# Performance work log

Hardware: AMD Instinct MI355X
Metric: run time of the kernel (lower is better)

## Reference

```python
import jax, jax.numpy as jnp
import numpy as np

LATENT_DIM = 64
K = 128


def setup_inputs() -> dict:
    key = jax.random.key(0)
    ks = jax.random.split(key, 7)
    B, T, N, d, k = 64, 1024, 1024, LATENT_DIM, K
    return {
        "review_seq": jax.random.normal(ks[0], (B, T, d), dtype=jnp.float32),
        "post_seq": jax.random.normal(ks[1], (B, N, d), dtype=jnp.float32),
        "Wl": jax.random.normal(ks[2], (d, d), dtype=jnp.float32) * 0.05,
        "Wr": jax.random.normal(ks[3], (k, d), dtype=jnp.float32) * 0.05,
        "Wp": jax.random.normal(ks[4], (k, d), dtype=jnp.float32) * 0.05,
        "whr": jax.random.normal(ks[5], (1, k), dtype=jnp.float32) * 0.05,
        "whp": jax.random.normal(ks[6], (1, k), dtype=jnp.float32) * 0.05,
    }


def reference(review_seq, post_seq, Wl, Wr, Wp, whr, whp):
    # L[b,t,n] = tanh(review @ Wl @ post^T)
    L = jnp.tanh(jnp.einsum('btd,dD,bnD->btn', review_seq, Wl, post_seq))
    # Hp[b,k,n] = tanh(Wp @ post^T + Wr @ review^T @ L)
    Hp = jnp.tanh(jnp.einsum('kd,bnd->bkn', Wp, post_seq)
                  + jnp.einsum('kd,btd,btn->bkn', Wr, review_seq, L))
    # Hr[b,k,t] = tanh(Wr @ review^T + Wp @ post^T @ L^T)
    Hr = jnp.tanh(jnp.einsum('kd,btd->bkt', Wr, review_seq)
                  + jnp.einsum('kd,bnd,btn->bkt', Wp, post_seq, L))
    # attention weights over post (n) and review (t) positions
    Ap = jax.nn.softmax(jnp.einsum('yk,bkn->bn', whp, Hp), axis=-1)
    Ar = jax.nn.softmax(jnp.einsum('yk,bkt->bt', whr, Hr), axis=-1)
    co_p = jnp.einsum('bnd,bn->bd', post_seq, Ap)
    co_r = jnp.einsum('btd,bt->bd', review_seq, Ar)
    return jnp.concatenate([co_p, co_r], axis=1)  # [B, 2*latent_dim]
```

## Files before the change

### kernel.cpp

```cpp
#include <hip/hip_runtime.h>
#include <hip/hip_bf16.h>


typedef __attribute__((ext_vector_type(8))) short bfrag;
typedef __attribute__((ext_vector_type(4))) float ffrag;

typedef const __attribute__((address_space(1))) unsigned GAS_U;
typedef __attribute__((address_space(3))) unsigned LAS_U;

__device__ __forceinline__ void gload16(const void* g, void* l) {
  __builtin_amdgcn_global_load_lds((GAS_U*)g, (LAS_U*)l, 16, 0, 0);
}

__device__ __forceinline__ unsigned short f2b(float f) {
  unsigned u = __builtin_bit_cast(unsigned, f);
  u += 0x7FFFu + ((u >> 16) & 1u);
  return (unsigned short)(u >> 16);
}
__device__ __forceinline__ float b2f(unsigned short h) {
  return __builtin_bit_cast(float, (unsigned)h << 16);
}
__device__ __forceinline__ float ftanh(float x) {
  float e = __builtin_amdgcn_exp2f(x * 2.88539008177792681f);
  return fmaf(-2.0f, __builtin_amdgcn_rcpf(e + 1.0f), 1.0f);
}
__device__ __forceinline__ unsigned cvtpk(float lo, float hi) {
  unsigned r;
  asm("v_cvt_pk_bf16_f32 %0, %1, %2" : "=v"(r) : "v"(lo), "v"(hi));
  return r;
}

#define MFMA(a, b, c) __builtin_amdgcn_mfma_f32_16x16x32_bf16((a), (b), (c), 0, 0, 0)


__global__ __launch_bounds__(256) void prep_kernel(
    const float* __restrict__ review, const float* __restrict__ post,
    const float* __restrict__ Wl, const float* __restrict__ Wr,
    const float* __restrict__ Wp,
    unsigned short* __restrict__ RWb, unsigned short* __restrict__ Rb,
    unsigned short* __restrict__ Pb, unsigned short* __restrict__ postb)
{
  const int chunk = blockIdx.x, b = blockIdx.y, side = blockIdx.z;
  const int tid = threadIdx.x, lane = tid & 63, w = tid >> 6;
  const int lr = lane & 15, lg = lane >> 4;
  const int r0 = chunk * 128;

  __shared__ __align__(16) unsigned short seqs[128][72];
  __shared__ __align__(16) unsigned short wgt[128][72];
  __shared__ __align__(16) unsigned short wlt[64][72];

  const float* seq = (side == 0) ? review : post;
#pragma unroll
  for (int jj = 0; jj < 8; ++jj) {
    int e = tid + jj * 256;
    int r = e >> 4, d4 = (e & 15) * 4;
    float4 v = *(const float4*)(seq + ((size_t)(b * 1024 + r0 + r)) * 64 + d4);
    unsigned lo = ((unsigned)f2b(v.y) << 16) | f2b(v.x);
    unsigned hi = ((unsigned)f2b(v.w) << 16) | f2b(v.z);
    *(uint2*)&seqs[r][d4] = make_uint2(lo, hi);
    if (side == 1)
      *(uint2*)(postb + ((size_t)(b * 1024 + r0 + r)) * 64 + d4) = make_uint2(lo, hi);
  }
  const float* wkd = (side == 0) ? Wr : Wp;
#pragma unroll
  for (int jj = 0; jj < 8; ++jj) {
    int e = tid + jj * 256;
    int k = e >> 4, d4 = (e & 15) * 4;
    float4 v = *(const float4*)(wkd + k * 64 + d4);
    unsigned lo = ((unsigned)f2b(v.y) << 16) | f2b(v.x);
    unsigned hi = ((unsigned)f2b(v.w) << 16) | f2b(v.z);
    *(uint2*)&wgt[k][d4] = make_uint2(lo, hi);
  }
  if (side == 0) {
    for (int i = tid; i < 64 * 64; i += 256) {
      int d = i >> 6, c = i & 63;
      wlt[c][d] = f2b(Wl[d * 64 + c]);
    }
  }
  __syncthreads();

  if (side == 0) {
    ffrag acc[2][4] = {};
#pragma unroll
    for (int ks = 0; ks < 2; ++ks)
#pragma unroll
      for (int is = 0; is < 4; ++is) {
        bfrag a = *(const bfrag*)&wlt[is * 16 + lr][ks * 32 + lg * 8];
#pragma unroll
        for (int tt = 0; tt < 2; ++tt) {
          bfrag bb = *(const bfrag*)&seqs[(w * 2 + tt) * 16 + lr][ks * 32 + lg * 8];
          acc[tt][is] = MFMA(a, bb, acc[tt][is]);
        }
      }
#pragma unroll
    for (int tt = 0; tt < 2; ++tt) {
      const int t = r0 + (w * 2 + tt) * 16 + lr;
      char* rowb = (char*)RWb + ((size_t)(b * 1024 + t)) * 128 + lg * 8;
#pragma unroll
      for (int is = 0; is < 4; ++is) {
        uint2 pkv;
        pkv.x = cvtpk(acc[tt][is][0], acc[tt][is][1]);
        pkv.y = cvtpk(acc[tt][is][2], acc[tt][is][3]);
        *(uint2*)(rowb + is * 32) = pkv;
      }
    }
  }
  {
    ffrag acc[2][8] = {};
#pragma unroll
    for (int ks = 0; ks < 2; ++ks)
#pragma unroll
      for (int tt = 0; tt < 2; ++tt) {
        bfrag a = *(const bfrag*)&seqs[(w * 2 + tt) * 16 + lr][ks * 32 + lg * 8];
#pragma unroll
        for (int kt = 0; kt < 8; ++kt) {
          bfrag bb = *(const bfrag*)&wgt[kt * 16 + lr][ks * 32 + lg * 8];
          acc[tt][kt] = MFMA(a, bb, acc[tt][kt]);
        }
      }
    char* dstb = (char*)((side == 0) ? Rb : Pb) + (size_t)b * 262144
                 + (size_t)(chunk * 4 + w) * 8192 + lg * 256 + lr * 16;
#pragma unroll
    for (int tt = 0; tt < 2; ++tt)
#pragma unroll
      for (int kt = 0; kt < 8; ++kt) {
        uint2 pkv;
        pkv.x = cvtpk(acc[tt][kt][0], acc[tt][kt][1]);
        pkv.y = cvtpk(acc[tt][kt][2], acc[tt][kt][3]);
        *(uint2*)(dstb + kt * 1024 + tt * 8) = pkv;
      }
  }
}

__global__ __launch_bounds__(256, 4) void hz_kernel(
    const unsigned short* __restrict__ RWb, const unsigned short* __restrict__ Rb,
    const unsigned short* __restrict__ Pb, const unsigned short* __restrict__ postb,
    const float* __restrict__ whp, const float* __restrict__ whr,
    float* __restrict__ zp, float* __restrict__ zr)
{
  const int orig = blockIdx.x;
  const int swz = (orig & 7) * 128 + (orig >> 3);
  const int strip = swz & 7, pair = swz >> 3;
  const int b = pair & 63, role = pair >> 6;
  const int s0 = strip * 128;
  const int tid = threadIdx.x, lane = tid & 63, w = tid >> 6;
  const int lr = lane & 15, lg = lane >> 4;

  const unsigned short* resident = role ? RWb : postb;
  const unsigned short* chunkseq = role ? postb : RWb;
  const unsigned short* coeff    = role ? Pb : Rb;
  const unsigned short* addterm  = role ? Rb : Pb;
  const float* wh                = role ? whr : whp;
  float* zout                    = role ? zr : zp;

  __shared__ __align__(16) char smem[24576];
  const int woff = w << 10;

  const int crow = tid >> 3, cslot = tid & 7;
  const char* csrc = (const char*)chunkseq + (size_t)b * 131072
                     + crow * 128 + ((cslot ^ (crow & 7)) << 4);
  const char* ksrc = (const char*)coeff + (size_t)b * 262144 + tid * 16;

  bfrag rb[2][2];
  {
    const char* rbase = (const char*)resident + ((size_t)(b * 1024 + s0)) * 128
                        + (w * 32 + lr) * 128 + lg * 16;
#pragma unroll
    for (int rs = 0; rs < 2; ++rs) {
      rb[0][rs] = *(const bfrag*)(rbase + rs * 2048);
      rb[1][rs] = *(const bfrag*)(rbase + rs * 2048 + 64);
    }
  }

  gload16(csrc, smem + woff);
  gload16(ksrc, smem + 8192 + woff);
  gload16(ksrc + 4096, smem + 8192 + 4096 + woff);
  __syncthreads();

  ffrag acc[2][8] = {};

#pragma unroll 1
  for (int tc = 0; tc < 32; ++tc) {
    const int cur = tc & 1, nb = cur ^ 1;
    if (tc < 31) {
      gload16(csrc + (size_t)(tc + 1) * 4096, smem + nb * 4096 + woff);
      gload16(ksrc + (size_t)(tc + 1) * 8192, smem + 8192 + nb * 8192 + woff);
      gload16(ksrc + (size_t)(tc + 1) * 8192 + 4096,
              smem + 8192 + nb * 8192 + 4096 + woff);
    }

    const char* rwc = smem + cur * 4096;
    uint2 pk[2][2];
#pragma unroll
    for (int ts = 0; ts < 2; ++ts) {
      ffrag la0 = {}, la1 = {};
#pragma unroll
      for (int ks = 0; ks < 2; ++ks) {
        const int arow = ts * 16 + lr;
        bfrag a = *(const bfrag*)(rwc + arow * 128 + (((ks * 4 + lg) ^ (arow & 7)) << 4));
        la0 = MFMA(a, rb[ks][0], la0);
        la1 = MFMA(a, rb[ks][1], la1);
      }
      pk[ts][0].x = cvtpk(ftanh(la0[0]), ftanh(la0[1]));
      pk[ts][0].y = cvtpk(ftanh(la0[2]), ftanh(la0[3]));
      pk[ts][1].x = cvtpk(ftanh(la1[0]), ftanh(la1[1]));
      pk[ts][1].y = cvtpk(ftanh(la1[2]), ftanh(la1[3]));
    }
    uint4 a0u; a0u.x = pk[0][0].x; a0u.y = pk[0][0].y; a0u.z = pk[1][0].x; a0u.w = pk[1][0].y;
    uint4 a1u; a1u.x = pk[0][1].x; a1u.y = pk[0][1].y; a1u.z = pk[1][1].x; a1u.w = pk[1][1].y;
    const bfrag af0 = __builtin_bit_cast(bfrag, a0u);
    const bfrag af1 = __builtin_bit_cast(bfrag, a1u);

    const char* rlc = smem + 8192 + cur * 8192 + lg * 256 + lr * 16;
#pragma unroll
    for (int kt = 0; kt < 8; ++kt) {
      bfrag bk = *(const bfrag*)(rlc + kt * 1024);
      acc[0][kt] = MFMA(af0, bk, acc[0][kt]);
      acc[1][kt] = MFMA(af1, bk, acc[1][kt]);
    }
    __syncthreads();
  }

  float whs[8];
#pragma unroll
  for (int kt = 0; kt < 8; ++kt) whs[kt] = wh[kt * 16 + lr];

  const char* abase = (const char*)addterm + (size_t)b * 262144
                      + (size_t)(strip * 4 + w) * 8192
                      + lg * 256 + lr * 16;
  float zs[2][4] = {};
#pragma unroll
  for (int rs = 0; rs < 2; ++rs)
#pragma unroll
    for (int kt = 0; kt < 8; ++kt) {
      uint2 av = *(const uint2*)(abase + kt * 1024 + rs * 8);
      const float whk = whs[kt];
      zs[rs][0] += whk * ftanh(acc[rs][kt][0] + b2f((unsigned short)(av.x & 0xFFFF)));
      zs[rs][1] += whk * ftanh(acc[rs][kt][1] + b2f((unsigned short)(av.x >> 16)));
      zs[rs][2] += whk * ftanh(acc[rs][kt][2] + b2f((unsigned short)(av.y & 0xFFFF)));
      zs[rs][3] += whk * ftanh(acc[rs][kt][3] + b2f((unsigned short)(av.y >> 16)));
    }
#pragma unroll
  for (int rs = 0; rs < 2; ++rs)
#pragma unroll
    for (int j = 0; j < 4; ++j) {
      float v = zs[rs][j];
      v += __shfl_xor(v, 1);
      v += __shfl_xor(v, 2);
      v += __shfl_xor(v, 4);
      v += __shfl_xor(v, 8);
      if (lr == 0)
        zout[(size_t)b * 1024 + s0 + w * 32 + rs * 16 + lg * 4 + j] = v;
    }
}

__global__ __launch_bounds__(1024) void final_kernel(
    const float* __restrict__ review, const float* __restrict__ post,
    const float* __restrict__ zp, const float* __restrict__ zr,
    float* __restrict__ out)
{
  const int b = blockIdx.x, side = blockIdx.y, tid = threadIdx.x;
  const int wid = tid >> 6, lane = tid & 63;
  __shared__ float zl[1024];
  __shared__ float red[16];
  __shared__ float cacc[16][64];

  const float* z = (side == 0) ? zp : zr;
  const float* seq = (side == 0) ? post : review;

  float v = z[(size_t)b * 1024 + tid];
  zl[tid] = v;
  float m = v;
#pragma unroll
  for (int off = 32; off; off >>= 1) m = fmaxf(m, __shfl_xor(m, off));
  if (lane == 0) red[wid] = m;
  __syncthreads();
  m = red[0];
#pragma unroll
  for (int i = 1; i < 16; ++i) m = fmaxf(m, red[i]);
  __syncthreads();

  float e = __expf(v - m);
  zl[tid] = e;
  float sm = e;
#pragma unroll
  for (int off = 32; off; off >>= 1) sm += __shfl_xor(sm, off);
  if (lane == 0) red[wid] = sm;
  __syncthreads();
  sm = red[0];
#pragma unroll
  for (int i = 1; i < 16; ++i) sm += red[i];
  const float inv = 1.0f / sm;

  const int d = lane;
  float a = 0.f;
  for (int n = wid * 64; n < wid * 64 + 64; ++n)
    a += zl[n] * seq[((size_t)(b * 1024 + n)) * 64 + d];
  cacc[wid][d] = a;
  __syncthreads();
  if (tid < 64) {
    float s = 0.f;
#pragma unroll
    for (int g = 0; g < 16; ++g) s += cacc[g][tid];
    out[b * 128 + side * 64 + tid] = s * inv;
  }
}

extern "C" void kernel_launch(void* const* d_in, const int* in_sizes, int n_in,
                              void* d_out, int out_size, void* d_ws, size_t ws_size,
                              hipStream_t stream) {
  const float* review = (const float*)d_in[0];
  const float* post   = (const float*)d_in[1];
  const float* Wl     = (const float*)d_in[2];
  const float* Wr     = (const float*)d_in[3];
  const float* Wp     = (const float*)d_in[4];
  const float* whr    = (const float*)d_in[5];
  const float* whp    = (const float*)d_in[6];
  float* out = (float*)d_out;

  char* ws = (char*)d_ws;
  unsigned short* RWb   = (unsigned short*)(ws);
  unsigned short* Rb    = (unsigned short*)(ws + (size_t)8  * 1048576);
  unsigned short* Pb    = (unsigned short*)(ws + (size_t)24 * 1048576);
  unsigned short* postb = (unsigned short*)(ws + (size_t)40 * 1048576);
  float* zp = (float*)(ws + (size_t)48 * 1048576);
  float* zr = (float*)(ws + (size_t)48 * 1048576 + 262144);

  prep_kernel<<<dim3(8, 64, 2), dim3(256), 0, stream>>>(
      review, post, Wl, Wr, Wp, RWb, Rb, Pb, postb);
  hz_kernel<<<dim3(1024), dim3(256), 0, stream>>>(
      RWb, Rb, Pb, postb, whp, whr, zp, zr);
  final_kernel<<<dim3(64, 2), dim3(1024), 0, stream>>>(
      review, post, zp, zr, out);
}
```

Baseline: 97.34 us.

## Fuse softmax-pooling into hz_kernel via last-block atomic counter; prescale tanh constant

Result: slower. 121.9 us (+25.2%).

```diff
diff --git a/kernel.cpp b/kernel.cpp
--- a/kernel.cpp
+++ b/kernel.cpp
@@ -7,6 +7,8 @@
 
 typedef const __attribute__((address_space(1))) unsigned GAS_U;
 typedef __attribute__((address_space(3))) unsigned LAS_U;
+
+#define TANH_SCALE 2.88539008177792681f
 
 __device__ __forceinline__ void gload16(const void* g, void* l) {
   __builtin_amdgcn_global_load_lds((GAS_U*)g, (LAS_U*)l, 16, 0, 0);
@@ -20,8 +22,8 @@
 __device__ __forceinline__ float b2f(unsigned short h) {
   return __builtin_bit_cast(float, (unsigned)h << 16);
 }
-__device__ __forceinline__ float ftanh(float x) {
-  float e = __builtin_amdgcn_exp2f(x * 2.88539008177792681f);
+__device__ __forceinline__ float ftanhe(float xs) {
+  float e = __builtin_amdgcn_exp2f(xs);
   return fmaf(-2.0f, __builtin_amdgcn_rcpf(e + 1.0f), 1.0f);
 }
 __device__ __forceinline__ unsigned cvtpk(float lo, float hi) {
@@ -67,14 +69,14 @@
     int e = tid + jj * 256;
     int k = e >> 4, d4 = (e & 15) * 4;
     float4 v = *(const float4*)(wkd + k * 64 + d4);
-    unsigned lo = ((unsigned)f2b(v.y) << 16) | f2b(v.x);
-    unsigned hi = ((unsigned)f2b(v.w) << 16) | f2b(v.z);
+    unsigned lo = ((unsigned)f2b(v.y * TANH_SCALE) << 16) | f2b(v.x * TANH_SCALE);
+    unsigned hi = ((unsigned)f2b(v.w * TANH_SCALE) << 16) | f2b(v.z * TANH_SCALE);
     *(uint2*)&wgt[k][d4] = make_uint2(lo, hi);
   }
   if (side == 0) {
     for (int i = tid; i < 64 * 64; i += 256) {
       int d = i >> 6, c = i & 63;
-      wlt[c][d] = f2b(Wl[d * 64 + c]);
+      wlt[c][d] = f2b(Wl[d * 64 + c] * TANH_SCALE);
     }
   }
   __syncthreads();
@@ -136,7 +138,9 @@
     const unsigned short* __restrict__ RWb, const unsigned short* __restrict__ Rb,
     const unsigned short* __restrict__ Pb, const unsigned short* __restrict__ postb,
     const float* __restrict__ whp, const float* __restrict__ whr,
-    float* __restrict__ zp, float* __restrict__ zr)
+    float* __restrict__ zp, float* __restrict__ zr,
+    const float* __restrict__ review, const float* __restrict__ post,
+    float* __restrict__ out, int* __restrict__ cnt)
 {
   const int orig = blockIdx.x;
   const int swz = (orig & 7) * 128 + (orig >> 3);
@@ -154,6 +158,7 @@
   float* zout                    = role ? zr : zp;
 
   __shared__ __align__(16) char smem[24576];
+  __shared__ int winflag;
   const int woff = w << 10;
 
   const int crow = tid >> 3, cslot = tid & 7;
@@ -201,10 +206,10 @@
         la0 = MFMA(a, rb[ks][0], la0);
         la1 = MFMA(a, rb[ks][1], la1);
       }
-      pk[ts][0].x = cvtpk(ftanh(la0[0]), ftanh(la0[1]));
-      pk[ts][0].y = cvtpk(ftanh(la0[2]), ftanh(la0[3]));
-      pk[ts][1].x = cvtpk(ftanh(la1[0]), ftanh(la1[1]));
-      pk[ts][1].y = cvtpk(ftanh(la1[2]), ftanh(la1[3]));
+      pk[ts][0].x = cvtpk(ftanhe(la0[0]), ftanhe(la0[1]));
+      pk[ts][0].y = cvtpk(ftanhe(la0[2]), ftanhe(la0[3]));
+      pk[ts][1].x = cvtpk(ftanhe(la1[0]), ftanhe(la1[1]));
+      pk[ts][1].y = cvtpk(ftanhe(la1[2]), ftanhe(la1[3]));
     }
     uint4 a0u; a0u.x = pk[0][0].x; a0u.y = pk[0][0].y; a0u.z = pk[1][0].x; a0u.w = pk[1][0].y;
     uint4 a1u; a1u.x = pk[0][1].x; a1u.y = pk[0][1].y; a1u.z = pk[1][1].x; a1u.w = pk[1][1].y;
@@ -235,10 +240,10 @@
     for (int kt = 0; kt < 8; ++kt) {
       uint2 av = *(const uint2*)(abase + kt * 1024 + rs * 8);
       const float whk = whs[kt];
-      zs[rs][0] += whk * ftanh(acc[rs][kt][0] + b2f((unsigned short)(av.x & 0xFFFF)));
-      zs[rs][1] += whk * ftanh(acc[rs][kt][1] + b2f((unsigned short)(av.x >> 16)));
-      zs[rs][2] += whk * ftanh(acc[rs][kt][2] + b2f((unsigned short)(av.y & 0xFFFF)));
-      zs[rs][3] += whk * ftanh(acc[rs][kt][3] + b2f((unsigned short)(av.y >> 16)));
+      zs[rs][0] += whk * ftanhe(acc[rs][kt][0] + b2f((unsigned short)(av.x & 0xFFFF)));
+      zs[rs][1] += whk * ftanhe(acc[rs][kt][1] + b2f((unsigned short)(av.x >> 16)));
+      zs[rs][2] += whk * ftanhe(acc[rs][kt][2] + b2f((unsigned short)(av.y & 0xFFFF)));
+      zs[rs][3] += whk * ftanhe(acc[rs][kt][3] + b2f((unsigned short)(av.y >> 16)));
     }
 #pragma unroll
   for (int rs = 0; rs < 2; ++rs)
@@ -252,57 +257,59 @@
       if (lr == 0)
         zout[(size_t)b * 1024 + s0 + w * 32 + rs * 16 + lg * 4 + j] = v;
     }
-}
-
-__global__ __launch_bounds__(1024) void final_kernel(
-    const float* __restrict__ review, const float* __restrict__ post,
-    const float* __restrict__ zp, const float* __restrict__ zr,
-    float* __restrict__ out)
-{
-  const int b = blockIdx.x, side = blockIdx.y, tid = threadIdx.x;
-  const int wid = tid >> 6, lane = tid & 63;
-  __shared__ float zl[1024];
-  __shared__ float red[16];
-  __shared__ float cacc[16][64];
-
-  const float* z = (side == 0) ? zp : zr;
-  const float* seq = (side == 0) ? post : review;
-
-  float v = z[(size_t)b * 1024 + tid];
-  zl[tid] = v;
-  float m = v;
-#pragma unroll
-  for (int off = 32; off; off >>= 1) m = fmaxf(m, __shfl_xor(m, off));
-  if (lane == 0) red[wid] = m;
-  __syncthreads();
-  m = red[0];
-#pragma unroll
-  for (int i = 1; i < 16; ++i) m = fmaxf(m, red[i]);
-  __syncthreads();
-
-  float e = __expf(v - m);
-  zl[tid] = e;
-  float sm = e;
-#pragma unroll
-  for (int off = 32; off; off >>= 1) sm += __shfl_xor(sm, off);
-  if (lane == 0) red[wid] = sm;
-  __syncthreads();
-  sm = red[0];
-#pragma unroll
-  for (int i = 1; i < 16; ++i) sm += red[i];
-  const float inv = 1.0f / sm;
-
-  const int d = lane;
-  float a = 0.f;
-  for (int n = wid * 64; n < wid * 64 + 64; ++n)
-    a += zl[n] * seq[((size_t)(b * 1024 + n)) * 64 + d];
-  cacc[wid][d] = a;
-  __syncthreads();
-  if (tid < 64) {
-    float s = 0.f;
-#pragma unroll
-    for (int g = 0; g < 16; ++g) s += cacc[g][tid];
-    out[b * 128 + side * 64 + tid] = s * inv;
+
+  __syncthreads();
+  if (tid == 0) {
+    __threadfence();
+    int old = atomicAdd(&cnt[role * 64 + b], 1);
+    winflag = (old == 7);
+  }
+  __syncthreads();
+  if (!winflag) return;
+  if (tid == 0) __threadfence();
+  __syncthreads();
+
+  {
+    float* zl  = (float*)smem;
+    float* red = (float*)(smem + 4096);
+    float* cac = (float*)(smem + 8192);
+    const float* seq = role ? review : post;
+
+    for (int i = tid; i < 1024; i += 256) zl[i] = zout[(size_t)b * 1024 + i];
+    __syncthreads();
+    float m = -3.4e38f;
+    for (int i = tid; i < 1024; i += 256) m = fmaxf(m, zl[i]);
+    red[tid] = m;
+    __syncthreads();
+    for (int s = 128; s > 0; s >>= 1) {
+      if (tid < s) red[tid] = fmaxf(red[tid], red[tid + s]);
+      __syncthreads();
+    }
+    m = red[0];
+    __syncthreads();
+    float sm = 0.f;
+    for (int i = tid; i < 1024; i += 256) {
+      float e = __expf(zl[i] - m);
+      zl[i] = e;
+      sm += e;
+    }
+    red[tid] = sm;
+    __syncthreads();
+    for (int s = 128; s > 0; s >>= 1) {
+      if (tid < s) red[tid] += red[tid + s];
+      __syncthreads();
+    }
+    const float inv = 1.0f / red[0];
+    __syncthreads();
+    const int d = tid & 63, g = tid >> 6;
+    float a = 0.f;
+    for (int n = g * 256; n < g * 256 + 256; ++n)
+      a += zl[n] * seq[((size_t)(b * 1024 + n)) * 64 + d];
+    cac[g * 64 + d] = a;
+    __syncthreads();
+    if (tid < 64)
+      out[b * 128 + role * 64 + tid] =
+          (cac[tid] + cac[64 + tid] + cac[128 + tid] + cac[192 + tid]) * inv;
   }
 }
 
@@ -325,11 +332,11 @@
   unsigned short* postb = (unsigned short*)(ws + (size_t)40 * 1048576);
   float* zp = (float*)(ws + (size_t)48 * 1048576);
   float* zr = (float*)(ws + (size_t)48 * 1048576 + 262144);
-
+  int*   cnt = (int*)(ws + (size_t)48 * 1048576 + 524288);
+
+  hipMemsetAsync(cnt, 0, 512, stream);
   prep_kernel<<<dim3(8, 64, 2), dim3(256), 0, stream>>>(
       review, post, Wl, Wr, Wp, RWb, Rb, Pb, postb);
   hz_kernel<<<dim3(1024), dim3(256), 0, stream>>>(
-      RWb, Rb, Pb, postb, whp, whr, zp, zr);
-  final_kernel<<<dim3(64, 2), dim3(1024), 0, stream>>>(
-      review, post, zp, zr, out);
-}
+      RWb, Rb, Pb, postb, whp, whr, zp, zr, review, post, out, cnt);
+}
```
